# Kernel optimization log

Hardware: AMD Instinct MI355X
Metric: run time of the kernel (lower is better)

## Reference

```python
import jax, jax.numpy as jnp
import numpy as np

N_NODES = 100000
N_IN = 256
N_OUT = 64
N_EDGES = 1600000


def setup_inputs() -> dict:
    key = jax.random.key(0)
    k_x, k_w, k_b, k_v, k_r, k_c = jax.random.split(key, 6)
    x = jax.random.normal(k_x, (N_NODES, N_IN), dtype=jnp.float32)
    W = jax.random.normal(k_w, (N_IN, N_OUT), dtype=jnp.float32) * (1.0 / np.sqrt(N_IN))
    b = jax.random.normal(k_b, (N_OUT,), dtype=jnp.float32) * 0.01
    adj_vals = jax.random.uniform(k_v, (N_EDGES,), dtype=jnp.float32)
    edge_rows = jax.random.randint(k_r, (N_EDGES,), 0, N_NODES, dtype=jnp.int32)
    edge_cols = jax.random.randint(k_c, (N_EDGES,), 0, N_NODES, dtype=jnp.int32)
    return {"x": x, "W": W, "b": b, "adj_vals": adj_vals,
            "edge_rows": edge_rows, "edge_cols": edge_cols}


def reference(x, W, b, adj_vals, edge_rows, edge_cols):
    # linear projection: [N, n_in] @ [n_in, n_out] + b -> [N, n_out]
    h = x @ W + b
    # sparse-dense matmul: out[i] = sum_e adj_vals[e] * h[edge_cols[e]] for edge_rows[e]==i
    msgs = h[edge_cols] * adj_vals[:, None]  # [E, n_out]
    out = jax.ops.segment_sum(msgs, edge_rows, num_segments=N_NODES)
    return out
```

## Files before the change

kernel.cpp:

```cpp
#include <hip/hip_runtime.h>


#include <stdint.h>

constexpr int KDIM = 256;
constexpr int MOUT = 64;

constexpr int RPB = 128;
constexpr int RPB_SHIFT = 7;
constexpr int MAXBUCK = 1024;
constexpr int CHUNK = 4096;
constexpr int COL_BITS = 20;
constexpr int COL_MASK = (1 << COL_BITS) - 1;
constexpr int SORT_CAP = 6144;
constexpr int HIST_BLOCKS = 256;

typedef __attribute__((ext_vector_type(8))) short short8v;
typedef __attribute__((ext_vector_type(4))) float f32x4;

__device__ __forceinline__ unsigned short f2bf(float f) {
  unsigned u = __float_as_uint(f);
  return (unsigned short)((u + 0x7fffu + ((u >> 16) & 1u)) >> 16);
}

__global__ __launch_bounds__(256)
void prep(const float* __restrict__ W, unsigned short* __restrict__ wt,
          const int* __restrict__ rows, int* __restrict__ bcnt, int E, int nbuck) {
  const int t = threadIdx.x;
  if ((int)blockIdx.x < 64) {
    int n = blockIdx.x;
    wt[n * KDIM + t] = f2bf(W[(size_t)t * MOUT + n]);
    return;
  }
  __shared__ int cnt[MAXBUCK];
  for (int i = t; i < nbuck; i += 256) cnt[i] = 0;
  __syncthreads();
  const int b0 = blockIdx.x - 64;
  for (int e = b0 * 256 + t; e < E; e += HIST_BLOCKS * 256)
    atomicAdd(&cnt[rows[e] >> RPB_SHIFT], 1);
  __syncthreads();
  for (int i = t; i < nbuck; i += 256)
    if (cnt[i]) atomicAdd(&bcnt[i], cnt[i]);
}

__global__ __launch_bounds__(1024)
void scan_buckets(const int* __restrict__ bcnt, int* __restrict__ bptr,
                  int* __restrict__ bcur, int nbuck, int E) {
  __shared__ int buf[1024];
  __shared__ int carry;
  const int t = threadIdx.x;
  if (t == 0) carry = 0;
  __syncthreads();
  for (int c0 = 0; c0 < nbuck; c0 += 1024) {
    int i = c0 + t;
    int x = (i < nbuck) ? bcnt[i] : 0;
    buf[t] = x;
    __syncthreads();
    for (int off = 1; off < 1024; off <<= 1) {
      int v = (t >= off) ? buf[t - off] : 0;
      __syncthreads();
      buf[t] += v;
      __syncthreads();
    }
    int incl = buf[t];
    int base = carry;
    if (i < nbuck) {
      int ex = base + incl - x;
      bptr[i] = ex;
      bcur[i] = ex;
    }
    __syncthreads();
    if (t == 1023) carry = base + incl;
    __syncthreads();
  }
  if (t == 0) bptr[nbuck] = E;
}

__global__ __launch_bounds__(256, 4)
void gemm_scatter(const float* __restrict__ x, const unsigned short* __restrict__ wt,
                  const float* __restrict__ bvec, unsigned short* __restrict__ h,
                  const int* __restrict__ rows, const int* __restrict__ cols,
                  const float* __restrict__ vals, int* __restrict__ bcur,
                  int2* __restrict__ sorted, int gemmBlocks, int N, int E, int nbuck) {
  __shared__ int lcnt[MAXBUCK];
  __shared__ int lbase[MAXBUCK];
  const int t = threadIdx.x;

  if ((int)blockIdx.x < gemmBlocks) {
    const int wave = t >> 6, lane = t & 63;
    const int lo = lane & 15, hi = lane >> 4;
    const int rowbase = blockIdx.x * 128 + wave * 32;

    float bias[4];
#pragma unroll
    for (int nt = 0; nt < 4; ++nt) bias[nt] = bvec[nt * 16 + lo];

    const float* xb[2];
#pragma unroll
    for (int mr = 0; mr < 2; ++mr) {
      int r = rowbase + mr * 16 + lo;
      if (r >= N) r = N - 1;
      xb[mr] = &x[(size_t)r * KDIM + hi * 8];
    }

    f32x4 acc[2][4] = {};
    float4 pa[2][2], pb[2][2];
#pragma unroll
    for (int mr = 0; mr < 2; ++mr) {
      pa[0][mr] = *reinterpret_cast<const float4*>(xb[mr]);
      pb[0][mr] = *reinterpret_cast<const float4*>(xb[mr] + 4);
    }

#pragma unroll
    for (int ks = 0; ks < 8; ++ks) {
      const int cs = ks & 1, ns = cs ^ 1;
      if (ks < 7) {
#pragma unroll
        for (int mr = 0; mr < 2; ++mr) {
          pa[ns][mr] = *reinterpret_cast<const float4*>(xb[mr] + (ks + 1) * 32);
          pb[ns][mr] = *reinterpret_cast<const float4*>(xb[mr] + (ks + 1) * 32 + 4);
        }
      }
      short8v bfr[4];
#pragma unroll
      for (int nt = 0; nt < 4; ++nt)
        bfr[nt] = *reinterpret_cast<const short8v*>(
            &wt[(size_t)(nt * 16 + lo) * KDIM + ks * 32 + hi * 8]);
#pragma unroll
      for (int mr = 0; mr < 2; ++mr) {
        float4 p0 = pa[cs][mr];
        float4 p1 = pb[cs][mr];
        short8v a;
        a[0] = (short)f2bf(p0.x); a[1] = (short)f2bf(p0.y);
        a[2] = (short)f2bf(p0.z); a[3] = (short)f2bf(p0.w);
        a[4] = (short)f2bf(p1.x); a[5] = (short)f2bf(p1.y);
        a[6] = (short)f2bf(p1.z); a[7] = (short)f2bf(p1.w);
#pragma unroll
        for (int nt = 0; nt < 4; ++nt)
          acc[mr][nt] = __builtin_amdgcn_mfma_f32_16x16x32_bf16(a, bfr[nt], acc[mr][nt], 0, 0, 0);
      }
    }

#pragma unroll
    for (int mr = 0; mr < 2; ++mr)
#pragma unroll
      for (int reg = 0; reg < 4; ++reg) {
        int row = rowbase + mr * 16 + hi * 4 + reg;
        if (row < N) {
#pragma unroll
          for (int nt = 0; nt < 4; ++nt)
            h[(size_t)row * MOUT + nt * 16 + lo] = f2bf(acc[mr][nt][reg] + bias[nt]);
        }
      }
    return;
  }

  const int cid = blockIdx.x - gemmBlocks;
  const int e0 = cid * CHUNK;
  const int e1 = min(e0 + CHUNK, E);

  for (int i = t; i < nbuck; i += 256) lcnt[i] = 0;
  __syncthreads();
  for (int e = e0 + t; e < e1; e += 256)
    atomicAdd(&lcnt[rows[e] >> RPB_SHIFT], 1);
  __syncthreads();
  for (int i = t; i < nbuck; i += 256) {
    int c = lcnt[i];
    lbase[i] = c ? atomicAdd(&bcur[i], c) : 0;
  }
  __syncthreads();
  for (int i = t; i < nbuck; i += 256) lcnt[i] = 0;
  __syncthreads();
  for (int e = e0 + t; e < e1; e += 256) {
    int r = rows[e];
    int b = r >> RPB_SHIFT;
    int lrow = r & (RPB - 1);
    int pos = lbase[b] + atomicAdd(&lcnt[b], 1);
    sorted[pos] = make_int2((lrow << COL_BITS) | cols[e], __float_as_int(vals[e]));
  }
}

__global__ __launch_bounds__(256)
void bucket_sort(int2* __restrict__ sorted, const int* __restrict__ bptr,
                 int* __restrict__ row_ptr, int* __restrict__ bflag,
                 int N, int E, int nbuck) {
  __shared__ int2 eds[SORT_CAP];
  __shared__ int lcnt[RPB];
  __shared__ int loff[RPB];
  __shared__ int lcur[RPB];
  const int t = threadIdx.x;
  const int b = blockIdx.x;
  const int s = bptr[b];
  const int e = bptr[b + 1];
  const int cnt = e - s;
  const int row0 = b << RPB_SHIFT;

  if (b == 0 && t == 0) row_ptr[N] = E;

  if (cnt > SORT_CAP) {
    if (t == 0) bflag[b] = 1;
    if (t < RPB && row0 + t < N) row_ptr[row0 + t] = s;
    return;
  }
  if (t == 0) bflag[b] = 0;

  if (t < RPB) lcnt[t] = 0;
  __syncthreads();
  for (int j = s + t; j < e; j += 256) {
    int2 p = sorted[j];
    eds[j - s] = p;
    atomicAdd(&lcnt[p.x >> COL_BITS], 1);
  }
  __syncthreads();
  if (t < RPB) loff[t] = lcnt[t];
  __syncthreads();
  for (int off = 1; off < RPB; off <<= 1) {
    int v = (t < RPB && t >= off) ? loff[t - off] : 0;
    __syncthreads();
    if (t < RPB) loff[t] += v;
    __syncthreads();
  }
  if (t < RPB) {
    int ex = loff[t] - lcnt[t];
    loff[t] = ex;
    lcur[t] = 0;
    int grow = row0 + t;
    if (grow < N) row_ptr[grow] = s + ex;
  }
  __syncthreads();
  for (int idx = t; idx < cnt; idx += 256) {
    int2 p = eds[idx];
    int lr = p.x >> COL_BITS;
    int pos = s + loff[lr] + atomicAdd(&lcur[lr], 1);
    sorted[pos] = p;
  }
}

__device__ __forceinline__ void edge_fma(float* acc, const unsigned short* h,
                                         int2 p, int part) {
  float v = __int_as_float(p.y);
  int col = p.x & COL_MASK;
  uint4 hv = *reinterpret_cast<const uint4*>(&h[(size_t)col * MOUT + part * 8]);
  acc[0] += v * __uint_as_float(hv.x << 16);
  acc[1] += v * __uint_as_float(hv.x & 0xffff0000u);
  acc[2] += v * __uint_as_float(hv.y << 16);
  acc[3] += v * __uint_as_float(hv.y & 0xffff0000u);
  acc[4] += v * __uint_as_float(hv.z << 16);
  acc[5] += v * __uint_as_float(hv.z & 0xffff0000u);
  acc[6] += v * __uint_as_float(hv.w << 16);
  acc[7] += v * __uint_as_float(hv.w & 0xffff0000u);
}

__global__ __launch_bounds__(256)
void reduce_rows(const unsigned short* __restrict__ h, const int2* __restrict__ sorted,
                 const int* __restrict__ row_ptr, const int* __restrict__ bptr,
                 const int* __restrict__ bflag, float* __restrict__ out, int N) {
  int row = (blockIdx.x * 256 + threadIdx.x) >> 6;
  if (row >= N) return;
  int lane = threadIdx.x & 63;
  int slot = lane >> 3;
  int part = lane & 7;
  int b = row >> RPB_SHIFT;
  int lrow = row & (RPB - 1);
  bool filt = bflag[b] != 0;

  float acc[8];
#pragma unroll
  for (int i = 0; i < 8; ++i) acc[i] = 0.f;

  if (!filt) {
    int s = row_ptr[row];
    int e = row_ptr[row + 1];
    int j = s + slot;
    for (; j + 8 < e; j += 16) {
      int2 p0 = sorted[j];
      int2 p1 = sorted[j + 8];
      float v0 = __int_as_float(p0.y);
      float v1 = __int_as_float(p1.y);
      uint4 h0 = *reinterpret_cast<const uint4*>(
          &h[(size_t)(p0.x & COL_MASK) * MOUT + part * 8]);
      uint4 h1 = *reinterpret_cast<const uint4*>(
          &h[(size_t)(p1.x & COL_MASK) * MOUT + part * 8]);
      acc[0] += v0 * __uint_as_float(h0.x << 16);
      acc[1] += v0 * __uint_as_float(h0.x & 0xffff0000u);
      acc[2] += v0 * __uint_as_float(h0.y << 16);
      acc[3] += v0 * __uint_as_float(h0.y & 0xffff0000u);
      acc[4] += v0 * __uint_as_float(h0.z << 16);
      acc[5] += v0 * __uint_as_float(h0.z & 0xffff0000u);
      acc[6] += v0 * __uint_as_float(h0.w << 16);
      acc[7] += v0 * __uint_as_float(h0.w & 0xffff0000u);
      acc[0] += v1 * __uint_as_float(h1.x << 16);
      acc[1] += v1 * __uint_as_float(h1.x & 0xffff0000u);
      acc[2] += v1 * __uint_as_float(h1.y << 16);
      acc[3] += v1 * __uint_as_float(h1.y & 0xffff0000u);
      acc[4] += v1 * __uint_as_float(h1.z << 16);
      acc[5] += v1 * __uint_as_float(h1.z & 0xffff0000u);
      acc[6] += v1 * __uint_as_float(h1.w << 16);
      acc[7] += v1 * __uint_as_float(h1.w & 0xffff0000u);
    }
    if (j < e) edge_fma(acc, h, sorted[j], part);
  } else {
    int s = bptr[b];
    int e = bptr[b + 1];
    for (int j = s + slot; j < e; j += 8) {
      int2 p = sorted[j];
      if ((p.x >> COL_BITS) != lrow) continue;
      edge_fma(acc, h, p, part);
    }
  }

#pragma unroll
  for (int m = 8; m <= 32; m <<= 1)
#pragma unroll
    for (int i = 0; i < 8; ++i)
      acc[i] += __shfl_xor(acc[i], m, 64);

  if (slot == 0) {
    float* op = &out[(size_t)row * MOUT + part * 8];
    *reinterpret_cast<float4*>(op)     = make_float4(acc[0], acc[1], acc[2], acc[3]);
    *reinterpret_cast<float4*>(op + 4) = make_float4(acc[4], acc[5], acc[6], acc[7]);
  }
}

__global__ __launch_bounds__(256)
void scatter_edges(const unsigned short* __restrict__ h, const float* __restrict__ vals,
                   const int* __restrict__ rows, const int* __restrict__ cols,
                   float* __restrict__ out, int E) {
  long long idx = (long long)blockIdx.x * blockDim.x + threadIdx.x;
  int e = (int)(idx >> 4);
  int part = (int)(idx & 15);
  if (e >= E) return;
  int r = rows[e];
  int c = cols[e];
  float v = vals[e];
  uint2 hv = *reinterpret_cast<const uint2*>(&h[(size_t)c * MOUT + part * 4]);
  float* op = &out[(size_t)r * MOUT + part * 4];
  atomicAdd(op + 0, v * __uint_as_float(hv.x << 16));
  atomicAdd(op + 1, v * __uint_as_float(hv.x & 0xffff0000u));
  atomicAdd(op + 2, v * __uint_as_float(hv.y << 16));
  atomicAdd(op + 3, v * __uint_as_float(hv.y & 0xffff0000u));
}

__global__ __launch_bounds__(256)
void wt_transpose(const float* __restrict__ W, unsigned short* __restrict__ wt) {
  int n = blockIdx.x;
  int k = threadIdx.x;
  wt[n * KDIM + k] = f2bf(W[(size_t)k * MOUT + n]);
}

static inline size_t align256(size_t x) { return (x + 255) & ~(size_t)255; }

extern "C" void kernel_launch(void* const* d_in, const int* in_sizes, int n_in,
                              void* d_out, int out_size, void* d_ws, size_t ws_size,
                              hipStream_t stream) {
  const float* x    = (const float*)d_in[0];
  const float* W    = (const float*)d_in[1];
  const float* bvec = (const float*)d_in[2];
  const float* vals = (const float*)d_in[3];
  const int* erows  = (const int*)d_in[4];
  const int* ecols  = (const int*)d_in[5];
  float* out = (float*)d_out;

  const int N = in_sizes[0] / KDIM;
  const int E = in_sizes[3];
  const int nbuck = (N + RPB - 1) / RPB;

  char* ws = (char*)d_ws;
  size_t off_h  = 0;
  size_t off_wt = align256(off_h + (size_t)N * MOUT * sizeof(short));
  size_t off_bp = align256(off_wt + (size_t)MOUT * KDIM * sizeof(short));
  size_t off_bc = align256(off_bp + (size_t)(nbuck + 1) * sizeof(int));
  size_t off_cu = align256(off_bc + (size_t)nbuck * sizeof(int));
  size_t off_bf = align256(off_cu + (size_t)nbuck * sizeof(int));
  size_t off_rp = align256(off_bf + (size_t)nbuck * sizeof(int));
  size_t off_sp = align256(off_rp + (size_t)(N + 1) * sizeof(int));
  size_t need   = off_sp + (size_t)E * sizeof(int2);

  unsigned short* h  = (unsigned short*)(ws + off_h);
  unsigned short* wt = (unsigned short*)(ws + off_wt);

  dim3 blk256(256);
  const int gemmBlocks = (N + 127) / 128;

  if (ws_size >= need && nbuck <= MAXBUCK && N < (1 << COL_BITS)) {
    int* bptr  = (int*)(ws + off_bp);
    int* bcnt  = (int*)(ws + off_bc);
    int* bcur  = (int*)(ws + off_cu);
    int* bflag = (int*)(ws + off_bf);
    int* row_ptr = (int*)(ws + off_rp);
    int2* sorted = (int2*)(ws + off_sp);

    hipMemsetAsync(bcnt, 0, (size_t)nbuck * sizeof(int), stream);
    prep<<<dim3(64 + HIST_BLOCKS), blk256, 0, stream>>>(W, wt, erows, bcnt, E, nbuck);
    scan_buckets<<<dim3(1), dim3(1024), 0, stream>>>(bcnt, bptr, bcur, nbuck, E);
    const int scatBlocks = (E + CHUNK - 1) / CHUNK;
    gemm_scatter<<<dim3(gemmBlocks + scatBlocks), blk256, 0, stream>>>(
        x, wt, bvec, h, erows, ecols, vals, bcur, sorted, gemmBlocks, N, E, nbuck);
    bucket_sort<<<dim3(nbuck), blk256, 0, stream>>>(sorted, bptr, row_ptr, bflag, N, E, nbuck);
    reduce_rows<<<dim3(((size_t)N * 64 + 255) / 256), blk256, 0, stream>>>(
        h, sorted, row_ptr, bptr, bflag, out, N);
  } else {
    wt_transpose<<<dim3(MOUT), blk256, 0, stream>>>(W, wt);
    gemm_scatter<<<dim3(gemmBlocks), blk256, 0, stream>>>(
        x, wt, bvec, h, erows, ecols, vals, (int*)wt, (int2*)h, gemmBlocks, N, E, nbuck);
    hipMemsetAsync(d_out, 0, (size_t)out_size * sizeof(float), stream);
    long long work = (long long)E * 16;
    scatter_edges<<<dim3((unsigned)((work + 255) / 256)), blk256, 0, stream>>>(h, vals, erows, ecols, out, E);
  }
}
```

Before: 134.9 us.

## Stage GEMM x tiles into LDS via async global_load_lds with swizzle

Result: faster. 129.2 us (-4.2%).

```diff
diff --git a/kernel.cpp b/kernel.cpp
--- a/kernel.cpp
+++ b/kernel.cpp
@@ -21,6 +21,12 @@
 __device__ __forceinline__ unsigned short f2bf(float f) {
   unsigned u = __float_as_uint(f);
   return (unsigned short)((u + 0x7fffu + ((u >> 16) & 1u)) >> 16);
+}
+
+__device__ __forceinline__ void async_ld16(const float* g, float* l) {
+  __builtin_amdgcn_global_load_lds(
+      (const __attribute__((address_space(1))) void*)g,
+      (__attribute__((address_space(3))) void*)l, 16, 0, 0);
 }
 
 __global__ __launch_bounds__(256)
@@ -82,54 +88,64 @@
                   const int* __restrict__ rows, const int* __restrict__ cols,
                   const float* __restrict__ vals, int* __restrict__ bcur,
                   int2* __restrict__ sorted, int gemmBlocks, int N, int E, int nbuck) {
-  __shared__ int lcnt[MAXBUCK];
-  __shared__ int lbase[MAXBUCK];
+  __shared__ __align__(16) char smem[32768];
   const int t = threadIdx.x;
 
   if ((int)blockIdx.x < gemmBlocks) {
+    auto xs = reinterpret_cast<float(*)[128][32]>(smem);
     const int wave = t >> 6, lane = t & 63;
     const int lo = lane & 15, hi = lane >> 4;
-    const int rowbase = blockIdx.x * 128 + wave * 32;
+    const int row0 = blockIdx.x * 128;
+    const int rowbase = row0 + wave * 32;
+
+    auto stage = [&](int kt, int b) {
+#pragma unroll
+      for (int i = 0; i < 4; ++i) {
+        int g = i * 256 + t;
+        int row = g >> 3, c = g & 7;
+        int csw = c ^ (row & 7);
+        int rr = row0 + row; if (rr >= N) rr = N - 1;
+        const float* src = &x[(size_t)rr * KDIM + kt * 32 + csw * 4];
+        float* dst = &xs[b][0][0] + (size_t)(i * 256 + (t & 192)) * 4;
+        async_ld16(src, dst);
+      }
+    };
 
     float bias[4];
 #pragma unroll
     for (int nt = 0; nt < 4; ++nt) bias[nt] = bvec[nt * 16 + lo];
 
-    const float* xb[2];
+    int go0[2], go1[2], lrr[2];
 #pragma unroll
     for (int mr = 0; mr < 2; ++mr) {
-      int r = rowbase + mr * 16 + lo;
-      if (r >= N) r = N - 1;
-      xb[mr] = &x[(size_t)r * KDIM + hi * 8];
+      int lr = wave * 32 + mr * 16 + lo;
+      lrr[mr] = lr;
+      go0[mr] = (((hi * 2)    ) ^ (lr & 7)) * 4;
+      go1[mr] = (((hi * 2) + 1) ^ (lr & 7)) * 4;
     }
 
     f32x4 acc[2][4] = {};
-    float4 pa[2][2], pb[2][2];
-#pragma unroll
-    for (int mr = 0; mr < 2; ++mr) {
-      pa[0][mr] = *reinterpret_cast<const float4*>(xb[mr]);
-      pb[0][mr] = *reinterpret_cast<const float4*>(xb[mr] + 4);
-    }
-
-#pragma unroll
-    for (int ks = 0; ks < 8; ++ks) {
-      const int cs = ks & 1, ns = cs ^ 1;
-      if (ks < 7) {
-#pragma unroll
-        for (int mr = 0; mr < 2; ++mr) {
-          pa[ns][mr] = *reinterpret_cast<const float4*>(xb[mr] + (ks + 1) * 32);
-          pb[ns][mr] = *reinterpret_cast<const float4*>(xb[mr] + (ks + 1) * 32 + 4);
-        }
+    short8v wfr[2][4];
+#pragma unroll
+    for (int nt = 0; nt < 4; ++nt)
+      wfr[0][nt] = *reinterpret_cast<const short8v*>(&wt[(size_t)(nt * 16 + lo) * KDIM + hi * 8]);
+    stage(0, 0);
+
+#pragma unroll
+    for (int kt = 0; kt < 8; ++kt) {
+      const int cb = kt & 1;
+      __syncthreads();
+      if (kt < 7) {
+        stage(kt + 1, cb ^ 1);
+#pragma unroll
+        for (int nt = 0; nt < 4; ++nt)
+          wfr[cb ^ 1][nt] = *reinterpret_cast<const short8v*>(
+              &wt[(size_t)(nt * 16 + lo) * KDIM + (kt + 1) * 32 + hi * 8]);
       }
-      short8v bfr[4];
-#pragma unroll
-      for (int nt = 0; nt < 4; ++nt)
-        bfr[nt] = *reinterpret_cast<const short8v*>(
-            &wt[(size_t)(nt * 16 + lo) * KDIM + ks * 32 + hi * 8]);
 #pragma unroll
       for (int mr = 0; mr < 2; ++mr) {
-        float4 p0 = pa[cs][mr];
-        float4 p1 = pb[cs][mr];
+        float4 p0 = *reinterpret_cast<const float4*>(&xs[cb][lrr[mr]][go0[mr]]);
+        float4 p1 = *reinterpret_cast<const float4*>(&xs[cb][lrr[mr]][go1[mr]]);
         short8v a;
         a[0] = (short)f2bf(p0.x); a[1] = (short)f2bf(p0.y);
         a[2] = (short)f2bf(p0.z); a[3] = (short)f2bf(p0.w);
@@ -137,7 +153,7 @@
         a[6] = (short)f2bf(p1.z); a[7] = (short)f2bf(p1.w);
 #pragma unroll
         for (int nt = 0; nt < 4; ++nt)
-          acc[mr][nt] = __builtin_amdgcn_mfma_f32_16x16x32_bf16(a, bfr[nt], acc[mr][nt], 0, 0, 0);
+          acc[mr][nt] = __builtin_amdgcn_mfma_f32_16x16x32_bf16(a, wfr[cb][nt], acc[mr][nt], 0, 0, 0);
       }
     }
 
@@ -155,6 +171,8 @@
     return;
   }
 
+  int* lcnt  = reinterpret_cast<int*>(smem);
+  int* lbase = lcnt + MAXBUCK;
   const int cid = blockIdx.x - gemmBlocks;
   const int e0 = cid * CHUNK;
   const int e1 = min(e0 + CHUNK, E);
```
